# Optimization experiments

Hardware: AMD Instinct MI355X
Metric: run time of the kernel (lower is better)

Reference implementation:

```python
import jax, jax.numpy as jnp
import numpy as np

B, S, T, IN, H = 16384, 336, 48, 5, 64  # batch, enc seq, horizon, features, hidden


def _lstm_cell(x, h, c, Wih, Whh, bih, bhh):
    # PyTorch gate order: i, f, g, o
    g = x @ Wih.T + h @ Whh.T + bih + bhh  # [B, 4H]
    i, f, gg, o = jnp.split(g, 4, axis=-1)
    i, f, o = jax.nn.sigmoid(i), jax.nn.sigmoid(f), jax.nn.sigmoid(o)
    c_new = f * c + i * jnp.tanh(gg)
    h_new = o * jnp.tanh(c_new)
    return h_new, c_new


def setup_inputs() -> dict:
    key = jax.random.key(0)
    ks = jax.random.split(key, 20)
    k = 1.0 / np.sqrt(H)

    def p(kk, shape):
        return jax.random.uniform(kk, shape, jnp.float32, -k, k)

    d = {"src": jax.random.normal(ks[0], (B, S, IN), jnp.float32)}
    d["enc_Wih0"] = p(ks[1], (4 * H, IN)); d["enc_Whh0"] = p(ks[2], (4 * H, H))
    d["enc_bih0"] = p(ks[3], (4 * H,));   d["enc_bhh0"] = p(ks[4], (4 * H,))
    d["enc_Wih1"] = p(ks[5], (4 * H, H)); d["enc_Whh1"] = p(ks[6], (4 * H, H))
    d["enc_bih1"] = p(ks[7], (4 * H,));   d["enc_bhh1"] = p(ks[8], (4 * H,))
    d["dec_Wih0"] = p(ks[9], (4 * H, 1)); d["dec_Whh0"] = p(ks[10], (4 * H, H))
    d["dec_bih0"] = p(ks[11], (4 * H,));  d["dec_bhh0"] = p(ks[12], (4 * H,))
    d["dec_Wih1"] = p(ks[13], (4 * H, H)); d["dec_Whh1"] = p(ks[14], (4 * H, H))
    d["dec_bih1"] = p(ks[15], (4 * H,));  d["dec_bhh1"] = p(ks[16], (4 * H,))
    d["fc_W"] = p(ks[17], (1, H)); d["fc_b"] = p(ks[18], (1,))
    return d


def reference(src, enc_Wih0, enc_Whh0, enc_bih0, enc_bhh0,
              enc_Wih1, enc_Whh1, enc_bih1, enc_bhh1,
              dec_Wih0, dec_Whh0, dec_bih0, dec_bhh0,
              dec_Wih1, dec_Whh1, dec_bih1, dec_bhh1,
              fc_W, fc_b):
    b = src.shape[0]
    z = jnp.zeros((b, H), src.dtype)

    # ---- Encoder: 2-layer LSTM over S timesteps (inference: no dropout) ----
    def enc_step(carry, x_t):
        h0, c0, h1, c1 = carry
        h0, c0 = _lstm_cell(x_t, h0, c0, enc_Wih0, enc_Whh0, enc_bih0, enc_bhh0)
        h1, c1 = _lstm_cell(h0, h1, c1, enc_Wih1, enc_Whh1, enc_bih1, enc_bhh1)
        return (h0, c0, h1, c1), None

    (h0, c0, h1, c1), _ = jax.lax.scan(enc_step, (z, z, z, z),
                                       jnp.swapaxes(src, 0, 1))  # [S,B,IN]

    dec_in0 = src[:, -1, 3:4]  # [B, 1] (feature index 3 of last timestep)

    def dec_step(carry, _):
        h0, c0, h1, c1, x = carry
        h0, c0 = _lstm_cell(x, h0, c0, dec_Wih0, dec_Whh0, dec_bih0, dec_bhh0)
        h1, c1 = _lstm_cell(h0, h1, c1, dec_Wih1, dec_Whh1, dec_bih1, dec_bhh1)
        pred = h1 @ fc_W.T + fc_b  # [B, 1]
        return (h0, c0, h1, c1, pred), pred

    _, preds = jax.lax.scan(dec_step, (h0, c0, h1, c1, dec_in0), None, length=T)
    return jnp.transpose(preds, (1, 0, 2))  # [B, T, 1]
```

## Files before the change

### kernel.cpp

```cpp
#include <hip/hip_runtime.h>
#include <stdint.h>

#define B_ 16384
#define S_ 336
#define T_ 48
#define IN_ 5
#define H_ 64

#define ROWS 32
#define NT   (ROWS / 16)
#define GP   (ROWS * 8)

typedef _Float16 f16;
typedef _Float16 f16x8 __attribute__((ext_vector_type(8)));
typedef float f32x4 __attribute__((ext_vector_type(4)));

#define LOG2E 1.44269504088896340736f

#define OFF_E0 0
#define OFF_E1 24576
#define OFF_D0 57344
#define OFF_D1 81920
#define OFF_BE0 114688
#define OFF_BE1 114944
#define OFF_BD0 115200
#define OFF_BD1 115456
#define OFF_FCW 115712
#define OFF_FCB 115776
#define WS_TOT  115777

__device__ __forceinline__ float sig2(float g) {
    return __builtin_amdgcn_rcpf(1.0f + __builtin_amdgcn_exp2f(g));
}
__device__ __forceinline__ float tanh2(float g) {
    return 1.0f - 2.0f * __builtin_amdgcn_rcpf(1.0f + __builtin_amdgcn_exp2f(g));
}
__device__ __forceinline__ float tanhc(float c) {
    return 1.0f - 2.0f * __builtin_amdgcn_rcpf(1.0f + __builtin_amdgcn_exp2f(c * (2.0f * LOG2E)));
}

__global__ void prep_kernel(
    const float* __restrict__ eWih0, const float* __restrict__ eWhh0,
    const float* __restrict__ ebih0, const float* __restrict__ ebhh0,
    const float* __restrict__ eWih1, const float* __restrict__ eWhh1,
    const float* __restrict__ ebih1, const float* __restrict__ ebhh1,
    const float* __restrict__ dWih0, const float* __restrict__ dWhh0,
    const float* __restrict__ dbih0, const float* __restrict__ dbhh0,
    const float* __restrict__ dWih1, const float* __restrict__ dWhh1,
    const float* __restrict__ dbih1, const float* __restrict__ dbhh1,
    const float* __restrict__ fcW,  const float* __restrict__ fcb,
    float* __restrict__ ws)
{
    int idx = blockIdx.x * blockDim.x + threadIdx.x;
    if (idx >= WS_TOT) return;
    float outv;
    if (idx < OFF_BE0) {
        int rel, nkt, xdim;
        const float *Wi, *Wh, *bi, *bh;
        if (idx < OFF_E1)      { rel = idx - OFF_E0; nkt = 3; xdim = IN_; Wi = eWih0; Wh = eWhh0; bi = ebih0; bh = ebhh0; }
        else if (idx < OFF_D0) { rel = idx - OFF_E1; nkt = 4; xdim = 64;  Wi = eWih1; Wh = eWhh1; bi = 0; bh = 0; }
        else if (idx < OFF_D1) { rel = idx - OFF_D0; nkt = 3; xdim = 1;   Wi = dWih0; Wh = dWhh0; bi = dbih0; bh = dbhh0; }
        else                   { rel = idx - OFF_D1; nkt = 4; xdim = 64;  Wi = dWih1; Wh = dWhh1; bi = 0; bh = 0; }
        int reg = rel & 3, pl = (rel >> 2) & 1, lane = (rel >> 3) & 63;
        int rest = rel >> 9;
        int kt = rest % nkt, mt = rest / nkt;
        int gp = mt * 16 + (lane & 15);
        int type = gp & 3;
        int j  = type * 64 + (gp >> 2);
        float sc = (type == 2) ? (2.0f * LOG2E) : (-LOG2E);
        union { f16 h2[2]; float f; } u_;
        #pragma unroll
        for (int h = 0; h < 2; ++h) {
            int k = kt * 32 + (lane >> 4) * 8 + reg * 2 + h;
            float v;
            if (nkt == 4)      v = (k < 64) ? Wi[j * 64 + k] : Wh[j * 64 + (k - 64)];
            else if (k < xdim) v = Wi[j * xdim + k];
            else if (k == 5)   v = bi[j] + bh[j];
            else if (k >= 32)  v = Wh[j * 64 + (k - 32)];
            else               v = 0.0f;
            v *= sc;
            f16 hi = (f16)v;
            u_.h2[h] = (pl == 0) ? hi : (f16)(v - (float)hi);
        }
        outv = u_.f;
    } else if (idx < OFF_FCW) {
        int rel = idx - OFF_BE0;
        int which = rel >> 8, gp = rel & 255;
        int type = gp & 3;
        int j = type * 64 + (gp >> 2);
        float sc = (type == 2) ? (2.0f * LOG2E) : (-LOG2E);
        const float *bi, *bh;
        if (which == 0)      { bi = ebih0; bh = ebhh0; }
        else if (which == 1) { bi = ebih1; bh = ebhh1; }
        else if (which == 2) { bi = dbih0; bh = dbhh0; }
        else                 { bi = dbih1; bh = dbhh1; }
        outv = (bi[j] + bh[j]) * sc;
    } else if (idx < OFF_FCB) {
        outv = fcW[idx - OFF_FCW];
    } else {
        outv = fcb[0];
    }
    ws[idx] = outv;
}

#define XBI(b,p,g,r)   ((((b)*2+(p))*4+(g))*GP + (r)*8)
#define HBI(b,p,k,g,r) (((((b)*2+(p))*2+(k))*4+(g))*GP + (r)*8)
#define XTOT (2*2*4*GP)
#define HHALF (2*2*4*GP)

#define MFMA(a,b,c) __builtin_amdgcn_mfma_f32_16x16x32_f16(a, b, c, 0, 0, 0)

__device__ __forceinline__ void stage_x5(f16* __restrict__ XB, int b, int r, const float* xv) {
    f16x8 ph, pl_;
    #pragma unroll
    for (int i = 0; i < 8; ++i) { ph[i] = (f16)0; pl_[i] = (f16)0; }
    #pragma unroll
    for (int i = 0; i < IN_; ++i) {
        f16 hh = (f16)xv[i]; ph[i] = hh; pl_[i] = (f16)(xv[i] - (float)hh);
    }
    ph[5] = (f16)1.0f;
    *(f16x8*)&XB[XBI(b,0,0,r)] = ph;
    *(f16x8*)&XB[XBI(b,1,0,r)] = pl_;
}
__device__ __forceinline__ void stage_x1(f16* __restrict__ XB, int b, int r, float v) {
    f16x8 ph, pl_;
    #pragma unroll
    for (int i = 0; i < 8; ++i) { ph[i] = (f16)0; pl_[i] = (f16)0; }
    f16 hh = (f16)v; ph[0] = hh; pl_[0] = (f16)(v - (float)hh);
    ph[5] = (f16)1.0f;
    *(f16x8*)&XB[XBI(b,0,0,r)] = ph;
    *(f16x8*)&XB[XBI(b,1,0,r)] = pl_;
}

__device__ __forceinline__ void layer0_only(
    int pX, int pH0r, int pH0w, int wave, int lane,
    const f16x8 (&wa)[7], float (&c0)[NT],
    const f16* __restrict__ XB, f16* __restrict__ H0B)
{
    const int g4 = lane >> 4, l15 = lane & 15;
    const int u = wave * 4 + g4;
    #pragma unroll
    for (int nt = 0; nt < NT; ++nt) {
        const int r = nt * 16 + l15;
        f16x8 xh  = *(const f16x8*)&XB [XBI(pX,0,g4,r)];
        f16x8 xl  = *(const f16x8*)&XB [XBI(pX,1,g4,r)];
        f16x8 hh0 = *(const f16x8*)&H0B[HBI(pH0r,0,0,g4,r)];
        f16x8 hl0 = *(const f16x8*)&H0B[HBI(pH0r,1,0,g4,r)];
        f16x8 hh1 = *(const f16x8*)&H0B[HBI(pH0r,0,1,g4,r)];
        f16x8 hl1 = *(const f16x8*)&H0B[HBI(pH0r,1,1,g4,r)];
        f32x4 z = {0.0f, 0.0f, 0.0f, 0.0f};
        z = MFMA(wa[0], xh,  z);
        z = MFMA(wa[0], xl,  z);
        z = MFMA(wa[1], hh0, z);
        z = MFMA(wa[1], hl0, z);
        z = MFMA(wa[2], hh1, z);
        z = MFMA(wa[2], hl1, z);
        float ig = sig2(z[0]), fg = sig2(z[1]);
        float gg = tanh2(z[2]), og = sig2(z[3]);
        float c = fmaf(fg, c0[nt], ig * gg);
        c0[nt] = c;
        float h = og * tanhc(c);
        f16 hh = (f16)h, hl = (f16)(h - (float)hh);
        H0B[HBI(pH0w,0,(u>>5),(u>>3)&3,r) + (u&7)] = hh;
        H0B[HBI(pH0w,1,(u>>5),(u>>3)&3,r) + (u&7)] = hl;
    }
}

template<bool DEC>
__device__ __forceinline__ void layer1_only(
    int pH0, int pH1r, int pH1w, int wave, int lane,
    const f16x8 (&wa)[7], const f32x4 b1, float (&c1)[NT],
    const f16* __restrict__ H0B, f16* __restrict__ H1B, float* __restrict__ H1F)
{
    const int g4 = lane >> 4, l15 = lane & 15;
    const int u = wave * 4 + g4;
    #pragma unroll
    for (int nt = 0; nt < NT; ++nt) {
        const int r = nt * 16 + l15;
        f16x8 hh0 = *(const f16x8*)&H0B[HBI(pH0,0,0,g4,r)];
        f16x8 hl0 = *(const f16x8*)&H0B[HBI(pH0,1,0,g4,r)];
        f16x8 hh1 = *(const f16x8*)&H0B[HBI(pH0,0,1,g4,r)];
        f16x8 hl1 = *(const f16x8*)&H0B[HBI(pH0,1,1,g4,r)];
        f16x8 gh0 = *(const f16x8*)&H1B[HBI(pH1r,0,0,g4,r)];
        f16x8 gl0 = *(const f16x8*)&H1B[HBI(pH1r,1,0,g4,r)];
        f16x8 gh1 = *(const f16x8*)&H1B[HBI(pH1r,0,1,g4,r)];
        f16x8 gl1 = *(const f16x8*)&H1B[HBI(pH1r,1,1,g4,r)];
        f32x4 a = b1;
        a = MFMA(wa[3], hh0, a);
        a = MFMA(wa[3], hl0, a);
        a = MFMA(wa[4], hh1, a);
        a = MFMA(wa[4], hl1, a);
        a = MFMA(wa[5], gh0, a);
        a = MFMA(wa[5], gl0, a);
        a = MFMA(wa[6], gh1, a);
        a = MFMA(wa[6], gl1, a);
        float ig = sig2(a[0]), fg = sig2(a[1]);
        float gg = tanh2(a[2]), og = sig2(a[3]);
        float c = fmaf(fg, c1[nt], ig * gg);
        c1[nt] = c;
        float h = og * tanhc(c);
        f16 hh = (f16)h, hl = (f16)(h - (float)hh);
        H1B[HBI(pH1w,0,(u>>5),(u>>3)&3,r) + (u&7)] = hh;
        H1B[HBI(pH1w,1,(u>>5),(u>>3)&3,r) + (u&7)] = hl;
        if (DEC) H1F[u * 33 + r] = h;
    }
}

__device__ __forceinline__ void enc_phase(
    int p, int wave, int lane,
    const f16x8 (&wa)[7], const f32x4 b1,
    float (&c0)[NT], float (&c1)[NT],
    const f16* __restrict__ XB, f16* __restrict__ H0B, f16* __restrict__ H1B)
{
    const int g4 = lane >> 4, l15 = lane & 15;
    const int q = p ^ 1;
    const int u = wave * 4 + g4;
    #pragma unroll
    for (int nt = 0; nt < NT; ++nt) {
        const int r = nt * 16 + l15;
        f16x8 hh0 = *(const f16x8*)&H0B[HBI(p,0,0,g4,r)];
        f16x8 hl0 = *(const f16x8*)&H0B[HBI(p,1,0,g4,r)];
        f16x8 hh1 = *(const f16x8*)&H0B[HBI(p,0,1,g4,r)];
        f16x8 hl1 = *(const f16x8*)&H0B[HBI(p,1,1,g4,r)];
        f16x8 gh0 = *(const f16x8*)&H1B[HBI(q,0,0,g4,r)];
        f16x8 gl0 = *(const f16x8*)&H1B[HBI(q,1,0,g4,r)];
        f16x8 gh1 = *(const f16x8*)&H1B[HBI(q,0,1,g4,r)];
        f16x8 gl1 = *(const f16x8*)&H1B[HBI(q,1,1,g4,r)];
        f16x8 xh  = *(const f16x8*)&XB [XBI(q,0,g4,r)];
        f16x8 xl  = *(const f16x8*)&XB [XBI(q,1,g4,r)];
        f32x4 a = b1;
        f32x4 z = {0.0f, 0.0f, 0.0f, 0.0f};
        a = MFMA(wa[3], hh0, a);  z = MFMA(wa[0], xh,  z);
        a = MFMA(wa[3], hl0, a);  z = MFMA(wa[0], xl,  z);
        a = MFMA(wa[4], hh1, a);  z = MFMA(wa[1], hh0, z);
        a = MFMA(wa[4], hl1, a);  z = MFMA(wa[1], hl0, z);
        a = MFMA(wa[5], gh0, a);  z = MFMA(wa[2], hh1, z);
        a = MFMA(wa[5], gl0, a);  z = MFMA(wa[2], hl1, z);
        a = MFMA(wa[6], gh1, a);
        a = MFMA(wa[6], gl1, a);
        float ia = sig2(a[0]), iz = sig2(z[0]);
        float fa = sig2(a[1]), fz = sig2(z[1]);
        float ga = tanh2(a[2]), gz = tanh2(z[2]);
        float oa = sig2(a[3]), oz = sig2(z[3]);
        float ca = fmaf(fa, c1[nt], ia * ga); c1[nt] = ca;
        float cz = fmaf(fz, c0[nt], iz * gz); c0[nt] = cz;
        float ha = oa * tanhc(ca);
        float hz = oz * tanhc(cz);
        f16 hah = (f16)ha, hal = (f16)(ha - (float)hah);
        f16 hzh = (f16)hz, hzl = (f16)(hz - (float)hzh);
        H1B[HBI(p,0,(u>>5),(u>>3)&3,r) + (u&7)] = hah;
        H1B[HBI(p,1,(u>>5),(u>>3)&3,r) + (u&7)] = hal;
        H0B[HBI(q,0,(u>>5),(u>>3)&3,r) + (u&7)] = hzh;
        H0B[HBI(q,1,(u>>5),(u>>3)&3,r) + (u&7)] = hzl;
    }
}

__global__ __launch_bounds__(1024) void lstm_kernel(
    const float* __restrict__ src, const float* __restrict__ ws,
    float* __restrict__ out)
{
    __shared__ __align__(16) f16 XB [XTOT];
    __shared__ __align__(16) f16 H0B[2*HHALF];
    __shared__ __align__(16) f16 H1B[2*HHALF];
    __shared__ float H1F[64*33];
    __shared__ float FCW[64];

    const int tid  = threadIdx.x;
    const int lane = tid & 63;
    const int wave = __builtin_amdgcn_readfirstlane(tid >> 6);
    const int g4   = lane >> 4;
    const int rowBase = blockIdx.x * ROWS;

    float c0[NT], c1[NT];
    #pragma unroll
    for (int nt = 0; nt < NT; ++nt) { c0[nt] = 0.0f; c1[nt] = 0.0f; }

    f16x8 wa[7];
    f32x4 b1;

    auto ldw = [&](int off0, int off1, int ob1) {
        #pragma unroll
        for (int kt = 0; kt < 3; ++kt)
            wa[kt] = *(const f16x8*)(ws + off0 + ((wave * 3 + kt) * 64 + lane) * 8);
        #pragma unroll
        for (int kt = 0; kt < 4; ++kt)
            wa[3 + kt] = *(const f16x8*)(ws + off1 + ((wave * 4 + kt) * 64 + lane) * 8);
        b1 = *(const f32x4*)(ws + ob1 + wave * 16 + g4 * 4);
    };
    ldw(OFF_E0, OFF_E1, OFF_BE1);

    for (int i = tid; i < XTOT; i += 1024) XB[i] = (f16)0;
    for (int i = tid; i < HHALF; i += 1024) { H0B[HHALF + i] = (f16)0; H1B[HHALF + i] = (f16)0; }
    if (tid < 64) FCW[tid] = ws[OFF_FCW + tid];
    const float fcbv = ws[OFF_FCB];

    const int xr = lane & (ROWS - 1);
    const float* sp = src + (size_t)(rowBase + xr) * (S_ * IN_);
    __syncthreads();

    if (wave == 15 && lane < ROWS) {
        float xv[IN_];
        #pragma unroll
        for (int i = 0; i < IN_; ++i) xv[i] = sp[i];
        stage_x5(XB, 0, lane, xv);
        #pragma unroll
        for (int i = 0; i < IN_; ++i) xv[i] = sp[IN_ + i];
        stage_x5(XB, 1, lane, xv);
    }
    __syncthreads();

    layer0_only(0, 1, 0, wave, lane, wa, c0, XB, H0B);
    __syncthreads();

    #pragma unroll 1
    for (int t = 0; t < S_ - 1; ++t) {
        const int p = t & 1;
        float xv[IN_];
        const bool pf = (wave == 15) && (lane < ROWS) && (t + 2 < S_);
        if (pf) {
            #pragma unroll
            for (int i = 0; i < IN_; ++i) xv[i] = sp[(t + 2) * IN_ + i];
        }
        enc_phase(p, wave, lane, wa, b1, c0, c1, XB, H0B, H1B);
        if (pf) stage_x5(XB, p, lane, xv);
        __syncthreads();
    }

    layer1_only<false>(1, 0, 1, wave, lane, wa, b1, c1, H0B, H1B, H1F);
    __syncthreads();

    ldw(OFF_D0, OFF_D1, OFF_BD1);
    if (wave == 15 && lane < ROWS) stage_x1(XB, 0, lane, sp[(S_ - 1) * IN_ + 3]);
    __syncthreads();

    #pragma unroll 1
    for (int t = 0; t < T_; ++t) {
        const int q = t & 1;
        layer0_only(q, q ^ 1, q, wave, lane, wa, c0, XB, H0B);
        __syncthreads();
        layer1_only<true>(q, q ^ 1, q, wave, lane, wa, b1, c1, H0B, H1B, H1F);
        __syncthreads();
        if (wave == 0 && lane < ROWS) {
            float pv = fcbv;
            #pragma unroll 4
            for (int k = 0; k < 64; ++k) pv = fmaf(FCW[k], H1F[k * 33 + lane], pv);
            out[(size_t)(rowBase + lane) * T_ + t] = pv;
            if (t + 1 < T_) stage_x1(XB, q ^ 1, lane, pv);
        }
        __syncthreads();
    }
}

extern "C" void kernel_launch(void* const* d_in, const int* in_sizes, int n_in,
                              void* d_out, int out_size, void* d_ws, size_t ws_size,
                              hipStream_t stream)
{
    const float* src = (const float*)d_in[0];
    float* ws  = (float*)d_ws;
    float* out = (float*)d_out;

    prep_kernel<<<(WS_TOT + 255) / 256, 256, 0, stream>>>(
        (const float*)d_in[1],  (const float*)d_in[2],
        (const float*)d_in[3],  (const float*)d_in[4],
        (const float*)d_in[5],  (const float*)d_in[6],
        (const float*)d_in[7],  (const float*)d_in[8],
        (const float*)d_in[9],  (const float*)d_in[10],
        (const float*)d_in[11], (const float*)d_in[12],
        (const float*)d_in[13], (const float*)d_in[14],
        (const float*)d_in[15], (const float*)d_in[16],
        (const float*)d_in[17], (const float*)d_in[18],
        ws);

    lstm_kernel<<<B_ / ROWS, 1024, 0, stream>>>(src, ws, out);
}
```

Before: 1.685 ms.

## Switch LSTM recurrence to 32x32x16 MFMA with 64 rows per block

Moves the per-step gate matmuls from 16x16x32 MFMA tiles to 32x32x16 tiles and raises rows per block from 32 to 64, remapping waves to gate tiles and row halves. Weights are stored only as an fp16 hi part instead of a hi/lo split, and layer-1 bias is folded into an extra MFMA against a one-hot vector. The goal is more useful work per barrier step and fewer blocks, at the cost of more registers, a different LDS layout, and lower weight precision.

After: 1.628 ms. -3.4%, faster.

```diff
diff --git a/kernel.cpp b/kernel.cpp
--- a/kernel.cpp
+++ b/kernel.cpp
@@ -7,27 +7,23 @@
 #define IN_ 5
 #define H_ 64
 
-#define ROWS 32
-#define NT   (ROWS / 16)
-#define GP   (ROWS * 8)
+#define ROWS 64
 
 typedef _Float16 f16;
 typedef _Float16 f16x8 __attribute__((ext_vector_type(8)));
-typedef float f32x4 __attribute__((ext_vector_type(4)));
+typedef float f32x16 __attribute__((ext_vector_type(16)));
 
 #define LOG2E 1.44269504088896340736f
 
+#define NKC0 5
+#define NKC1 9
 #define OFF_E0 0
-#define OFF_E1 24576
-#define OFF_D0 57344
-#define OFF_D1 81920
-#define OFF_BE0 114688
-#define OFF_BE1 114944
-#define OFF_BD0 115200
-#define OFF_BD1 115456
-#define OFF_FCW 115712
-#define OFF_FCB 115776
-#define WS_TOT  115777
+#define OFF_E1 10240
+#define OFF_D0 28672
+#define OFF_D1 38912
+#define OFF_FCW 57344
+#define OFF_FCB 57408
+#define WS_TOT  57409
 
 __device__ __forceinline__ float sig2(float g) {
     return __builtin_amdgcn_rcpf(1.0f + __builtin_amdgcn_exp2f(g));
@@ -54,47 +50,47 @@
     int idx = blockIdx.x * blockDim.x + threadIdx.x;
     if (idx >= WS_TOT) return;
     float outv;
-    if (idx < OFF_BE0) {
-        int rel, nkt, xdim;
-        const float *Wi, *Wh, *bi, *bh;
-        if (idx < OFF_E1)      { rel = idx - OFF_E0; nkt = 3; xdim = IN_; Wi = eWih0; Wh = eWhh0; bi = ebih0; bh = ebhh0; }
-        else if (idx < OFF_D0) { rel = idx - OFF_E1; nkt = 4; xdim = 64;  Wi = eWih1; Wh = eWhh1; bi = 0; bh = 0; }
-        else if (idx < OFF_D1) { rel = idx - OFF_D0; nkt = 3; xdim = 1;   Wi = dWih0; Wh = dWhh0; bi = dbih0; bh = dbhh0; }
-        else                   { rel = idx - OFF_D1; nkt = 4; xdim = 64;  Wi = dWih1; Wh = dWhh1; bi = 0; bh = 0; }
-        int reg = rel & 3, pl = (rel >> 2) & 1, lane = (rel >> 3) & 63;
-        int rest = rel >> 9;
-        int kt = rest % nkt, mt = rest / nkt;
-        int gp = mt * 16 + (lane & 15);
-        int type = gp & 3;
-        int j  = type * 64 + (gp >> 2);
+    if (idx < OFF_FCW) {
+        int off, nkc, which;
+        if (idx < OFF_E1)      { off = OFF_E0; nkc = NKC0; which = 0; }
+        else if (idx < OFF_D0) { off = OFF_E1; nkc = NKC1; which = 1; }
+        else if (idx < OFF_D1) { off = OFF_D0; nkc = NKC0; which = 2; }
+        else                   { off = OFF_D1; nkc = NKC1; which = 3; }
+        int rel = idx - off;
+        int w = rel & 3, lane = (rel >> 2) & 63;
+        int rest = rel >> 8;
+        int kc = rest % nkc, gt = rest / nkc;
+        int gr = lane & 31;
+        int q = gr >> 2, type = gr & 3;
+        int j = type * 64 + gt * 8 + q;
         float sc = (type == 2) ? (2.0f * LOG2E) : (-LOG2E);
         union { f16 h2[2]; float f; } u_;
         #pragma unroll
-        for (int h = 0; h < 2; ++h) {
-            int k = kt * 32 + (lane >> 4) * 8 + reg * 2 + h;
-            float v;
-            if (nkt == 4)      v = (k < 64) ? Wi[j * 64 + k] : Wh[j * 64 + (k - 64)];
-            else if (k < xdim) v = Wi[j * xdim + k];
-            else if (k == 5)   v = bi[j] + bh[j];
-            else if (k >= 32)  v = Wh[j * 64 + (k - 32)];
-            else               v = 0.0f;
-            v *= sc;
-            f16 hi = (f16)v;
-            u_.h2[h] = (pl == 0) ? hi : (f16)(v - (float)hi);
+        for (int hf = 0; hf < 2; ++hf) {
+            int kl = (lane >> 5) * 8 + w * 2 + hf;
+            float v = 0.0f;
+            if (which == 0) {
+                if (kc == 0) {
+                    if (kl < IN_)      v = eWih0[j * IN_ + kl];
+                    else if (kl == 5)  v = ebih0[j] + ebhh0[j];
+                } else                   v = eWhh0[j * 64 + (kc - 1) * 16 + kl];
+            } else if (which == 1) {
+                if (kc < 4)            v = eWih1[j * 64 + kc * 16 + kl];
+                else if (kc < 8)       v = eWhh1[j * 64 + (kc - 4) * 16 + kl];
+                else if (kl == 0)      v = ebih1[j] + ebhh1[j];
+            } else if (which == 2) {
+                if (kc == 0) {
+                    if (kl == 0)       v = dWih0[j];
+                    else if (kl == 5)  v = dbih0[j] + dbhh0[j];
+                } else                   v = dWhh0[j * 64 + (kc - 1) * 16 + kl];
+            } else {
+                if (kc < 4)            v = dWih1[j * 64 + kc * 16 + kl];
+                else if (kc < 8)       v = dWhh1[j * 64 + (kc - 4) * 16 + kl];
+                else if (kl == 0)      v = dbih1[j] + dbhh1[j];
+            }
+            u_.h2[hf] = (f16)(v * sc);
         }
         outv = u_.f;
-    } else if (idx < OFF_FCW) {
-        int rel = idx - OFF_BE0;
-        int which = rel >> 8, gp = rel & 255;
-        int type = gp & 3;
-        int j = type * 64 + (gp >> 2);
-        float sc = (type == 2) ? (2.0f * LOG2E) : (-LOG2E);
-        const float *bi, *bh;
-        if (which == 0)      { bi = ebih0; bh = ebhh0; }
-        else if (which == 1) { bi = ebih1; bh = ebhh1; }
-        else if (which == 2) { bi = dbih0; bh = dbhh0; }
-        else                 { bi = dbih1; bh = dbhh1; }
-        outv = (bi[j] + bh[j]) * sc;
     } else if (idx < OFF_FCB) {
         outv = fcW[idx - OFF_FCW];
     } else {
@@ -103,156 +99,149 @@
     ws[idx] = outv;
 }
 
-#define XBI(b,p,g,r)   ((((b)*2+(p))*4+(g))*GP + (r)*8)
-#define HBI(b,p,k,g,r) (((((b)*2+(p))*2+(k))*4+(g))*GP + (r)*8)
-#define XTOT (2*2*4*GP)
-#define HHALF (2*2*4*GP)
-
-#define MFMA(a,b,c) __builtin_amdgcn_mfma_f32_16x16x32_f16(a, b, c, 0, 0, 0)
+__device__ __forceinline__ int xbi(int b, int pl, int hf, int row) {
+    return ((((b * 2 + pl) * 2 + hf) * 64) + row) * 8;
+}
+__device__ __forceinline__ int hbi(int b, int pl, int kc, int hf, int row) {
+    return (((((b * 2 + pl) * 4 + kc) * 2 + hf) * 64) + row) * 8;
+}
+#define XTOT  (2*2*2*64*8)
+#define HTOT  (2*2*4*2*64*8)
+#define HHALF (2*4*2*64*8)
+#define PLSTR (4*2*64*8)
+
+#define MFMA32(a,b,c) __builtin_amdgcn_mfma_f32_32x32x16_f16(a, b, c, 0, 0, 0)
 
 __device__ __forceinline__ void stage_x5(f16* __restrict__ XB, int b, int r, const float* xv) {
-    f16x8 ph, pl_;
-    #pragma unroll
-    for (int i = 0; i < 8; ++i) { ph[i] = (f16)0; pl_[i] = (f16)0; }
+    f16x8 ph = {}, pl_ = {}, zz = {};
     #pragma unroll
     for (int i = 0; i < IN_; ++i) {
         f16 hh = (f16)xv[i]; ph[i] = hh; pl_[i] = (f16)(xv[i] - (float)hh);
     }
     ph[5] = (f16)1.0f;
-    *(f16x8*)&XB[XBI(b,0,0,r)] = ph;
-    *(f16x8*)&XB[XBI(b,1,0,r)] = pl_;
+    *(f16x8*)&XB[xbi(b,0,0,r)] = ph;
+    *(f16x8*)&XB[xbi(b,0,1,r)] = zz;
+    *(f16x8*)&XB[xbi(b,1,0,r)] = pl_;
+    *(f16x8*)&XB[xbi(b,1,1,r)] = zz;
 }
 __device__ __forceinline__ void stage_x1(f16* __restrict__ XB, int b, int r, float v) {
-    f16x8 ph, pl_;
-    #pragma unroll
-    for (int i = 0; i < 8; ++i) { ph[i] = (f16)0; pl_[i] = (f16)0; }
+    f16x8 ph = {}, pl_ = {}, zz = {};
     f16 hh = (f16)v; ph[0] = hh; pl_[0] = (f16)(v - (float)hh);
     ph[5] = (f16)1.0f;
-    *(f16x8*)&XB[XBI(b,0,0,r)] = ph;
-    *(f16x8*)&XB[XBI(b,1,0,r)] = pl_;
+    *(f16x8*)&XB[xbi(b,0,0,r)] = ph;
+    *(f16x8*)&XB[xbi(b,0,1,r)] = zz;
+    *(f16x8*)&XB[xbi(b,1,0,r)] = pl_;
+    *(f16x8*)&XB[xbi(b,1,1,r)] = zz;
+}
+
+__device__ __forceinline__ void act_store(
+    float gi, float gf, float gg_, float go, float& c, int qi,
+    int gt, int hf, int row, int b, f16* __restrict__ H, float* __restrict__ H1F)
+{
+    float ig = sig2(gi), fg = sig2(gf);
+    float gg = tanh2(gg_), og = sig2(go);
+    float cc = fmaf(fg, c, ig * gg);
+    c = cc;
+    float h = og * tanhc(cc);
+    f16 hh = (f16)h, hl = (f16)(h - (float)hh);
+    int u = gt * 8 + 2 * qi + hf;
+    int base = hbi(b, 0, u >> 4, (u >> 3) & 1, row) + (u & 7);
+    H[base] = hh;
+    H[base + PLSTR] = hl;
+    if (H1F) H1F[u * 65 + row] = h;
 }
 
 __device__ __forceinline__ void layer0_only(
-    int pX, int pH0r, int pH0w, int wave, int lane,
-    const f16x8 (&wa)[7], float (&c0)[NT],
+    int pX, int pH0r, int pH0w, int gt, int hf, int row,
+    const f16x8 (&wa0)[NKC0], float (&c0)[4],
     const f16* __restrict__ XB, f16* __restrict__ H0B)
 {
-    const int g4 = lane >> 4, l15 = lane & 15;
-    const int u = wave * 4 + g4;
-    #pragma unroll
-    for (int nt = 0; nt < NT; ++nt) {
-        const int r = nt * 16 + l15;
-        f16x8 xh  = *(const f16x8*)&XB [XBI(pX,0,g4,r)];
-        f16x8 xl  = *(const f16x8*)&XB [XBI(pX,1,g4,r)];
-        f16x8 hh0 = *(const f16x8*)&H0B[HBI(pH0r,0,0,g4,r)];
-        f16x8 hl0 = *(const f16x8*)&H0B[HBI(pH0r,1,0,g4,r)];
-        f16x8 hh1 = *(const f16x8*)&H0B[HBI(pH0r,0,1,g4,r)];
-        f16x8 hl1 = *(const f16x8*)&H0B[HBI(pH0r,1,1,g4,r)];
-        f32x4 z = {0.0f, 0.0f, 0.0f, 0.0f};
-        z = MFMA(wa[0], xh,  z);
-        z = MFMA(wa[0], xl,  z);
-        z = MFMA(wa[1], hh0, z);
-        z = MFMA(wa[1], hl0, z);
-        z = MFMA(wa[2], hh1, z);
-        z = MFMA(wa[2], hl1, z);
-        float ig = sig2(z[0]), fg = sig2(z[1]);
-        float gg = tanh2(z[2]), og = sig2(z[3]);
-        float c = fmaf(fg, c0[nt], ig * gg);
-        c0[nt] = c;
-        float h = og * tanhc(c);
-        f16 hh = (f16)h, hl = (f16)(h - (float)hh);
-        H0B[HBI(pH0w,0,(u>>5),(u>>3)&3,r) + (u&7)] = hh;
-        H0B[HBI(pH0w,1,(u>>5),(u>>3)&3,r) + (u&7)] = hl;
-    }
+    f32x16 z = {};
+    #pragma unroll
+    for (int kc = 0; kc < 4; ++kc) {
+        f16x8 hh = *(const f16x8*)&H0B[hbi(pH0r,0,kc,hf,row)];
+        f16x8 hl = *(const f16x8*)&H0B[hbi(pH0r,1,kc,hf,row)];
+        z = MFMA32(wa0[1+kc], hh, z);
+        z = MFMA32(wa0[1+kc], hl, z);
+    }
+    {
+        f16x8 xh = *(const f16x8*)&XB[xbi(pX,0,hf,row)];
+        f16x8 xl = *(const f16x8*)&XB[xbi(pX,1,hf,row)];
+        z = MFMA32(wa0[0], xh, z);
+        z = MFMA32(wa0[0], xl, z);
+    }
+    #pragma unroll
+    for (int qi = 0; qi < 4; ++qi)
+        act_store(z[4*qi], z[4*qi+1], z[4*qi+2], z[4*qi+3], c0[qi], qi,
+                  gt, hf, row, pH0w, H0B, nullptr);
 }
 
 template<bool DEC>
 __device__ __forceinline__ void layer1_only(
-    int pH0, int pH1r, int pH1w, int wave, int lane,
-    const f16x8 (&wa)[7], const f32x4 b1, float (&c1)[NT],
+    int pH0, int pH1r, int pH1w, int gt, int hf, int row,
+    const f16x8 (&wa1)[NKC1], f16x8 bvec, float (&c1)[4],
     const f16* __restrict__ H0B, f16* __restrict__ H1B, float* __restrict__ H1F)
 {
-    const int g4 = lane >> 4, l15 = lane & 15;
-    const int u = wave * 4 + g4;
-    #pragma unroll
-    for (int nt = 0; nt < NT; ++nt) {
-        const int r = nt * 16 + l15;
-        f16x8 hh0 = *(const f16x8*)&H0B[HBI(pH0,0,0,g4,r)];
-        f16x8 hl0 = *(const f16x8*)&H0B[HBI(pH0,1,0,g4,r)];
-        f16x8 hh1 = *(const f16x8*)&H0B[HBI(pH0,0,1,g4,r)];
-        f16x8 hl1 = *(const f16x8*)&H0B[HBI(pH0,1,1,g4,r)];
-        f16x8 gh0 = *(const f16x8*)&H1B[HBI(pH1r,0,0,g4,r)];
-        f16x8 gl0 = *(const f16x8*)&H1B[HBI(pH1r,1,0,g4,r)];
-        f16x8 gh1 = *(const f16x8*)&H1B[HBI(pH1r,0,1,g4,r)];
-        f16x8 gl1 = *(const f16x8*)&H1B[HBI(pH1r,1,1,g4,r)];
-        f32x4 a = b1;
-        a = MFMA(wa[3], hh0, a);
-        a = MFMA(wa[3], hl0, a);
-        a = MFMA(wa[4], hh1, a);
-        a = MFMA(wa[4], hl1, a);
-        a = MFMA(wa[5], gh0, a);
-        a = MFMA(wa[5], gl0, a);
-        a = MFMA(wa[6], gh1, a);
-        a = MFMA(wa[6], gl1, a);
-        float ig = sig2(a[0]), fg = sig2(a[1]);
-        float gg = tanh2(a[2]), og = sig2(a[3]);
-        float c = fmaf(fg, c1[nt], ig * gg);
-        c1[nt] = c;
-        float h = og * tanhc(c);
-        f16 hh = (f16)h, hl = (f16)(h - (float)hh);
-        H1B[HBI(pH1w,0,(u>>5),(u>>3)&3,r) + (u&7)] = hh;
-        H1B[HBI(pH1w,1,(u>>5),(u>>3)&3,r) + (u&7)] = hl;
-        if (DEC) H1F[u * 33 + r] = h;
-    }
+    f32x16 a = {};
+    a = MFMA32(wa1[8], bvec, a);
+    #pragma unroll
+    for (int kc = 0; kc < 4; ++kc) {
+        f16x8 hh = *(const f16x8*)&H0B[hbi(pH0,0,kc,hf,row)];
+        f16x8 hl = *(const f16x8*)&H0B[hbi(pH0,1,kc,hf,row)];
+        a = MFMA32(wa1[kc], hh, a);
+        a = MFMA32(wa1[kc], hl, a);
+    }
+    #pragma unroll
+    for (int kc = 0; kc < 4; ++kc) {
+        f16x8 gh = *(const f16x8*)&H1B[hbi(pH1r,0,kc,hf,row)];
+        f16x8 gl = *(const f16x8*)&H1B[hbi(pH1r,1,kc,hf,row)];
+        a = MFMA32(wa1[4+kc], gh, a);
+        a = MFMA32(wa1[4+kc], gl, a);
+    }
+    #pragma unroll
+    for (int qi = 0; qi < 4; ++qi)
+        act_store(a[4*qi], a[4*qi+1], a[4*qi+2], a[4*qi+3], c1[qi], qi,
+                  gt, hf, row, pH1w, H1B, DEC ? H1F : nullptr);
 }
 
 __device__ __forceinline__ void enc_phase(
-    int p, int wave, int lane,
-    const f16x8 (&wa)[7], const f32x4 b1,
-    float (&c0)[NT], float (&c1)[NT],
+    int p, int gt, int hf, int row,
+    const f16x8 (&wa0)[NKC0], const f16x8 (&wa1)[NKC1], f16x8 bvec,
+    float (&c0)[4], float (&c1)[4],
     const f16* __restrict__ XB, f16* __restrict__ H0B, f16* __restrict__ H1B)
 {
-    const int g4 = lane >> 4, l15 = lane & 15;
     const int q = p ^ 1;
-    const int u = wave * 4 + g4;
-    #pragma unroll
-    for (int nt = 0; nt < NT; ++nt) {
-        const int r = nt * 16 + l15;
-        f16x8 hh0 = *(const f16x8*)&H0B[HBI(p,0,0,g4,r)];
-        f16x8 hl0 = *(const f16x8*)&H0B[HBI(p,1,0,g4,r)];
-        f16x8 hh1 = *(const f16x8*)&H0B[HBI(p,0,1,g4,r)];
-        f16x8 hl1 = *(const f16x8*)&H0B[HBI(p,1,1,g4,r)];
-        f16x8 gh0 = *(const f16x8*)&H1B[HBI(q,0,0,g4,r)];
-        f16x8 gl0 = *(const f16x8*)&H1B[HBI(q,1,0,g4,r)];
-        f16x8 gh1 = *(const f16x8*)&H1B[HBI(q,0,1,g4,r)];
-        f16x8 gl1 = *(const f16x8*)&H1B[HBI(q,1,1,g4,r)];
-        f16x8 xh  = *(const f16x8*)&XB [XBI(q,0,g4,r)];
-        f16x8 xl  = *(const f16x8*)&XB [XBI(q,1,g4,r)];
-        f32x4 a = b1;
-        f32x4 z = {0.0f, 0.0f, 0.0f, 0.0f};
-        a = MFMA(wa[3], hh0, a);  z = MFMA(wa[0], xh,  z);
-        a = MFMA(wa[3], hl0, a);  z = MFMA(wa[0], xl,  z);
-        a = MFMA(wa[4], hh1, a);  z = MFMA(wa[1], hh0, z);
-        a = MFMA(wa[4], hl1, a);  z = MFMA(wa[1], hl0, z);
-        a = MFMA(wa[5], gh0, a);  z = MFMA(wa[2], hh1, z);
-        a = MFMA(wa[5], gl0, a);  z = MFMA(wa[2], hl1, z);
-        a = MFMA(wa[6], gh1, a);
-        a = MFMA(wa[6], gl1, a);
-        float ia = sig2(a[0]), iz = sig2(z[0]);
-        float fa = sig2(a[1]), fz = sig2(z[1]);
-        float ga = tanh2(a[2]), gz = tanh2(z[2]);
-        float oa = sig2(a[3]), oz = sig2(z[3]);
-        float ca = fmaf(fa, c1[nt], ia * ga); c1[nt] = ca;
-        float cz = fmaf(fz, c0[nt], iz * gz); c0[nt] = cz;
-        float ha = oa * tanhc(ca);
-        float hz = oz * tanhc(cz);
-        f16 hah = (f16)ha, hal = (f16)(ha - (float)hah);
-        f16 hzh = (f16)hz, hzl = (f16)(hz - (float)hzh);
-        H1B[HBI(p,0,(u>>5),(u>>3)&3,r) + (u&7)] = hah;
-        H1B[HBI(p,1,(u>>5),(u>>3)&3,r) + (u&7)] = hal;
-        H0B[HBI(q,0,(u>>5),(u>>3)&3,r) + (u&7)] = hzh;
-        H0B[HBI(q,1,(u>>5),(u>>3)&3,r) + (u&7)] = hzl;
-    }
+    f32x16 a = {};
+    f32x16 z = {};
+    a = MFMA32(wa1[8], bvec, a);
+    #pragma unroll
+    for (int kc = 0; kc < 4; ++kc) {
+        f16x8 hh = *(const f16x8*)&H0B[hbi(p,0,kc,hf,row)];
+        f16x8 hl = *(const f16x8*)&H0B[hbi(p,1,kc,hf,row)];
+        a = MFMA32(wa1[kc], hh, a);
+        a = MFMA32(wa1[kc], hl, a);
+        z = MFMA32(wa0[1+kc], hh, z);
+        z = MFMA32(wa0[1+kc], hl, z);
+    }
+    {
+        f16x8 xh = *(const f16x8*)&XB[xbi(q,0,hf,row)];
+        f16x8 xl = *(const f16x8*)&XB[xbi(q,1,hf,row)];
+        z = MFMA32(wa0[0], xh, z);
+        z = MFMA32(wa0[0], xl, z);
+    }
+    #pragma unroll
+    for (int kc = 0; kc < 4; ++kc) {
+        f16x8 gh = *(const f16x8*)&H1B[hbi(q,0,kc,hf,row)];
+        f16x8 gl = *(const f16x8*)&H1B[hbi(q,1,kc,hf,row)];
+        a = MFMA32(wa1[4+kc], gh, a);
+        a = MFMA32(wa1[4+kc], gl, a);
+        act_store(z[4*kc], z[4*kc+1], z[4*kc+2], z[4*kc+3], c0[kc], kc,
+                  gt, hf, row, q, H0B, nullptr);
+    }
+    #pragma unroll
+    for (int qi = 0; qi < 4; ++qi)
+        act_store(a[4*qi], a[4*qi+1], a[4*qi+2], a[4*qi+3], c1[qi], qi,
+                  gt, hf, row, p, H1B, nullptr);
 }
 
 __global__ __launch_bounds__(1024) void lstm_kernel(
@@ -260,45 +249,46 @@
     float* __restrict__ out)
 {
     __shared__ __align__(16) f16 XB [XTOT];
-    __shared__ __align__(16) f16 H0B[2*HHALF];
-    __shared__ __align__(16) f16 H1B[2*HHALF];
-    __shared__ float H1F[64*33];
+    __shared__ __align__(16) f16 H0B[HTOT];
+    __shared__ __align__(16) f16 H1B[HTOT];
+    __shared__ float H1F[64 * 65];
     __shared__ float FCW[64];
 
     const int tid  = threadIdx.x;
     const int lane = tid & 63;
     const int wave = __builtin_amdgcn_readfirstlane(tid >> 6);
-    const int g4   = lane >> 4;
+    const int gt   = wave >> 1;
+    const int rt   = wave & 1;
+    const int hf   = lane >> 5;
+    const int row  = rt * 32 + (lane & 31);
     const int rowBase = blockIdx.x * ROWS;
 
-    float c0[NT], c1[NT];
-    #pragma unroll
-    for (int nt = 0; nt < NT; ++nt) { c0[nt] = 0.0f; c1[nt] = 0.0f; }
-
-    f16x8 wa[7];
-    f32x4 b1;
-
-    auto ldw = [&](int off0, int off1, int ob1) {
-        #pragma unroll
-        for (int kt = 0; kt < 3; ++kt)
-            wa[kt] = *(const f16x8*)(ws + off0 + ((wave * 3 + kt) * 64 + lane) * 8);
-        #pragma unroll
-        for (int kt = 0; kt < 4; ++kt)
-            wa[3 + kt] = *(const f16x8*)(ws + off1 + ((wave * 4 + kt) * 64 + lane) * 8);
-        b1 = *(const f32x4*)(ws + ob1 + wave * 16 + g4 * 4);
+    float c0[4], c1[4];
+    #pragma unroll
+    for (int i = 0; i < 4; ++i) { c0[i] = 0.0f; c1[i] = 0.0f; }
+
+    f16x8 wa0[NKC0], wa1[NKC1];
+    f16x8 bvec = {};
+    if (hf == 0) bvec[0] = (f16)1.0f;
+
+    auto ldw = [&](int off0, int off1) {
+        #pragma unroll
+        for (int kc = 0; kc < NKC0; ++kc)
+            wa0[kc] = *(const f16x8*)(ws + off0 + ((gt * NKC0 + kc) * 64 + lane) * 4);
+        #pragma unroll
+        for (int kc = 0; kc < NKC1; ++kc)
+            wa1[kc] = *(const f16x8*)(ws + off1 + ((gt * NKC1 + kc) * 64 + lane) * 4);
     };
-    ldw(OFF_E0, OFF_E1, OFF_BE1);
-
-    for (int i = tid; i < XTOT; i += 1024) XB[i] = (f16)0;
+    ldw(OFF_E0, OFF_E1);
+
     for (int i = tid; i < HHALF; i += 1024) { H0B[HHALF + i] = (f16)0; H1B[HHALF + i] = (f16)0; }
     if (tid < 64) FCW[tid] = ws[OFF_FCW + tid];
     const float fcbv = ws[OFF_FCB];
 
-    const int xr = lane & (ROWS - 1);
-    const float* sp = src + (size_t)(rowBase + xr) * (S_ * IN_);
-    __syncthreads();
-
-    if (wave == 15 && lane < ROWS) {
+    const float* sp = src + (size_t)(rowBase + lane) * (S_ * IN_);
+    __syncthreads();
+
+    if (wave == 15) {
         float xv[IN_];
         #pragma unroll
         for (int i = 0; i < IN_; ++i) xv[i] = sp[i];
@@ -309,41 +299,41 @@
     }
     __syncthreads();
 
-    layer0_only(0, 1, 0, wave, lane, wa, c0, XB, H0B);
+    layer0_only(0, 1, 0, gt, hf, row, wa0, c0, XB, H0B);
     __syncthreads();
 
     #pragma unroll 1
     for (int t = 0; t < S_ - 1; ++t) {
         const int p = t & 1;
         float xv[IN_];
-        const bool pf = (wave == 15) && (lane < ROWS) && (t + 2 < S_);
+        const bool pf = (wave == 15) && (t + 2 < S_);
         if (pf) {
             #pragma unroll
             for (int i = 0; i < IN_; ++i) xv[i] = sp[(t + 2) * IN_ + i];
         }
-        enc_phase(p, wave, lane, wa, b1, c0, c1, XB, H0B, H1B);
+        enc_phase(p, gt, hf, row, wa0, wa1, bvec, c0, c1, XB, H0B, H1B);
         if (pf) stage_x5(XB, p, lane, xv);
         __syncthreads();
     }
 
-    layer1_only<false>(1, 0, 1, wave, lane, wa, b1, c1, H0B, H1B, H1F);
-    __syncthreads();
-
-    ldw(OFF_D0, OFF_D1, OFF_BD1);
-    if (wave == 15 && lane < ROWS) stage_x1(XB, 0, lane, sp[(S_ - 1) * IN_ + 3]);
+    layer1_only<false>(1, 0, 1, gt, hf, row, wa1, bvec, c1, H0B, H1B, H1F);
+    __syncthreads();
+
+    ldw(OFF_D0, OFF_D1);
+    if (wave == 15) stage_x1(XB, 0, lane, sp[(S_ - 1) * IN_ + 3]);
     __syncthreads();
 
     #pragma unroll 1
     for (int t = 0; t < T_; ++t) {
         const int q = t & 1;
-        layer0_only(q, q ^ 1, q, wave, lane, wa, c0, XB, H0B);
+        layer0_only(q, q ^ 1, q, gt, hf, row, wa0, c0, XB, H0B);
         __syncthreads();
-        layer1_only<true>(q, q ^ 1, q, wave, lane, wa, b1, c1, H0B, H1B, H1F);
+        layer1_only<true>(q, q ^ 1, q, gt, hf, row, wa1, bvec, c1, H0B, H1B, H1F);
         __syncthreads();
-        if (wave == 0 && lane < ROWS) {
+        if (wave == 0) {
             float pv = fcbv;
-            #pragma unroll 4
-            for (int k = 0; k < 64; ++k) pv = fmaf(FCW[k], H1F[k * 33 + lane], pv);
+            #pragma unroll 8
+            for (int k = 0; k < 64; ++k) pv = fmaf(FCW[k], H1F[k * 65 + lane], pv);
             out[(size_t)(rowBase + lane) * T_ + t] = pv;
             if (t + 1 < T_) stage_x1(XB, q ^ 1, lane, pv);
         }
```
